# Optimization experiments

Measured on AMD Instinct MI355X. Metric: run time of the kernel, lower is better.

Reference implementation:

```python
import jax, jax.numpy as jnp
import numpy as np

R = 8
EPS = 1e-08
EPSS = 1e-12


def _diff_x(x, r):
    left = x[:, :, r:2 * r + 1]
    middle = x[:, :, 2 * r + 1:] - x[:, :, :-2 * r - 1]
    right = x[:, :, -1:] - x[:, :, -2 * r - 1:-r - 1]
    return jnp.concatenate([left, middle, right], axis=2)


def _diff_y(x, r):
    left = x[:, :, :, r:2 * r + 1]
    middle = x[:, :, :, 2 * r + 1:] - x[:, :, :, :-2 * r - 1]
    right = x[:, :, :, -1:] - x[:, :, :, -2 * r - 1:-r - 1]
    return jnp.concatenate([left, middle, right], axis=3)


def box_filter(x, r):
    # cumsum-based (2r+1)x(2r+1) box sum with clamped borders (matches torch BoxFilter)
    return _diff_y(jnp.cumsum(_diff_x(jnp.cumsum(x, axis=2), r), axis=3), r)


def bilinear_resize(x, H, W):
    # F.interpolate(mode='bilinear', align_corners=True) for NCHW
    n, c, h, w = x.shape
    ys = jnp.linspace(0.0, h - 1.0, H)
    xs = jnp.linspace(0.0, w - 1.0, W)
    y0 = jnp.floor(ys).astype(jnp.int32)
    x0 = jnp.floor(xs).astype(jnp.int32)
    y1 = jnp.minimum(y0 + 1, h - 1)
    x1 = jnp.minimum(x0 + 1, w - 1)
    wy = (ys - y0).astype(x.dtype)[None, None, :, None]
    wx = (xs - x0).astype(x.dtype)[None, None, None, :]
    rows = jnp.take(x, y0, axis=2) * (1.0 - wy) + jnp.take(x, y1, axis=2) * wy
    return jnp.take(rows, x0, axis=3) * (1.0 - wx) + jnp.take(rows, x1, axis=3) * wx


def setup_inputs() -> dict:
    key = jax.random.key(0)
    k1, k2, k3, k4 = jax.random.split(key, 4)
    return {
        "lr_x": jax.random.normal(k1, (4, 3, 256, 256), dtype=jnp.float32),
        "lr_y": jax.random.normal(k2, (4, 3, 256, 256), dtype=jnp.float32),
        "hr_x": jax.random.normal(k3, (4, 3, 1024, 1024), dtype=jnp.float32),
        "l_a": jax.random.uniform(k4, (4, 3, 256, 256), dtype=jnp.float32),
    }


def reference(lr_x, lr_y, hr_x, l_a):
    n, c, h, w = lr_x.shape
    _, _, hh, wh = hr_x.shape
    dt = lr_x.dtype

    N = box_filter(jnp.ones((1, 1, h, w), dtype=dt), R)  # local window counts

    l_a = jnp.abs(l_a) + EPSS
    l_t = l_a / jnp.sum(l_a)

    mean_a = box_filter(l_a) if False else box_filter(l_a, R) / N
    mean_a2xy = box_filter(l_a * l_a * lr_x * lr_y, R) / N
    mean_tax = box_filter(l_t * l_a * lr_x, R) / N
    mean_ay = box_filter(l_a * lr_y, R) / N
    mean_a2x2 = box_filter(l_a * l_a * lr_x * lr_x, R) / N
    mean_ax = box_filter(l_a * lr_x, R) / N

    temp = jnp.abs(mean_a2x2 - N * mean_tax * mean_ax)
    A = (mean_a2xy - N * mean_tax * mean_ay) / (temp + EPS)
    b = (mean_ay - A * mean_ax) / mean_a

    A = box_filter(A, R) / N
    b = box_filter(b, R) / N

    mean_A = bilinear_resize(A, hh, wh)
    mean_b = bilinear_resize(b, hh, wh)
    return (mean_A * hr_x + mean_b).astype(jnp.float32)
```

## Files before the change

kernel.cpp:

```cpp
#include <hip/hip_runtime.h>

#define RAD 8
#define HH 256
#define WW 256
#define NC 12
#define PS (HH*WW)
#define SCALE (255.0f/1023.0f)

#define NREG 68
#define NMID 52
#define NCEN 36
#define INP  69
#define HP   53
#define CP   37
#define HS   (NREG*HP)

__device__ __forceinline__ int swz(int b) { return (b & 7) * 96 + (b >> 3); }

__global__ __launch_bounds__(256) void k_reduce(const float* __restrict__ la,
                                                float* __restrict__ partials) {
    int tid = threadIdx.x;
    __shared__ float ls[4];
    const float4* p4 = (const float4*)la;
    int base = blockIdx.x * 2048 + tid;
    float s = 0.f;
    #pragma unroll
    for (int i = 0; i < 8; i++) {
        float4 v = p4[base + i * 256];
        s += (fabsf(v.x) + 1e-12f) + (fabsf(v.y) + 1e-12f) +
             (fabsf(v.z) + 1e-12f) + (fabsf(v.w) + 1e-12f);
    }
    for (int off = 32; off > 0; off >>= 1) s += __shfl_down(s, off, 64);
    int lane = tid & 63, wid = tid >> 6;
    if (lane == 0) ls[wid] = s;
    __syncthreads();
    if (tid == 0) partials[blockIdx.x] = ls[0] + ls[1] + ls[2] + ls[3];
}

__global__ __launch_bounds__(512, 1) void k_fused(const float* __restrict__ la,
                                                  const float* __restrict__ lx,
                                                  const float* __restrict__ ly,
                                                  const float* __restrict__ hrx,
                                                  const float* __restrict__ partials,
                                                  float* __restrict__ out) {
    __shared__ float sIn[3 * NREG * INP];
    __shared__ float sH[6 * HS];
    __shared__ float sred[8];
    float* inA  = sIn;
    float* inX  = sIn + NREG * INP;
    float* inY  = sIn + 2 * NREG * INP;
    float* Abuf = inA;
    float* Bbuf = inX;
    float* HAb  = inY;
    float* HBb  = inY + NMID * CP;
    float* mAb  = sH;
    float* mBb  = sH + NCEN * CP;

    int tid = threadIdx.x;
    int b  = swz(blockIdx.x);
    int p  = b >> 6;
    int t  = b & 63;
    int ti = t >> 3, tj = t & 7;
    int I0 = ti << 7, J0 = tj << 7;
    int Lr0 = max(0, (I0 * 255) / 1023 - 1);
    int Lc0 = max(0, (J0 * 255) / 1023 - 1);

    {
        float x = (tid < 96) ? partials[tid] : 0.f;
        for (int off = 32; off > 0; off >>= 1) x += __shfl_down(x, off, 64);
        if ((tid & 63) == 0) sred[tid >> 6] = x;
    }

    int r0g = Lr0 - 16, c0g = Lc0 - 16;
    const int plane = p * PS;
    for (unsigned idx = tid; idx < (unsigned)(NREG * NREG); idx += 512u) {
        int r = (int)(idx / 68u), c = (int)(idx % 68u);
        int gr = r0g + r, gc = c0g + c;
        float va = 0.f, vx = 0.f, vy = 0.f;
        if (gr >= 0 && gr < HH && gc >= 0 && gc < WW) {
            int off = plane + gr * WW + gc;
            va = fabsf(la[off]) + 1e-12f;
            vx = lx[off];
            vy = ly[off];
        }
        int w = r * INP + c;
        inA[w] = va; inX[w] = vx; inY[w] = vy;
    }
    __syncthreads();
    float invS = 1.0f / (sred[0] + sred[1] + sred[2] + sred[3] +
                         sred[4] + sred[5] + sred[6] + sred[7]);

    for (unsigned job = tid; job < 272u; job += 512u) {
        int r = (int)(job % 68u), strip = (int)(job / 68u);
        const float* rA = inA + r * INP;
        const float* rX = inX + r * INP;
        const float* rY = inY + r * INP;
        float* w0 = sH + r * HP;
        int c0 = strip * 13;
        float s0 = 0, s1 = 0, s2 = 0, s3 = 0, s4 = 0, s5 = 0;
        #pragma unroll
        for (int c = 0; c < 17; c++) {
            float a = rA[c0 + c], x = rX[c0 + c], y = rY[c0 + c];
            float ax = a * x, ay = a * y;
            s0 += a; s1 += ax; s2 += ay; s3 += a * ax; s4 += ax * ax; s5 += ax * ay;
        }
        w0[c0] = s0; w0[HS + c0] = s1; w0[2 * HS + c0] = s2;
        w0[3 * HS + c0] = s3; w0[4 * HS + c0] = s4; w0[5 * HS + c0] = s5;
        for (int jm = c0 + 1; jm <= c0 + 12; jm++) {
            float a = rA[jm + 16], x = rX[jm + 16], y = rY[jm + 16];
            float ax = a * x, ay = a * y;
            s0 += a; s1 += ax; s2 += ay; s3 += a * ax; s4 += ax * ax; s5 += ax * ay;
            a = rA[jm - 1]; x = rX[jm - 1]; y = rY[jm - 1];
            ax = a * x; ay = a * y;
            s0 -= a; s1 -= ax; s2 -= ay; s3 -= a * ax; s4 -= ax * ax; s5 -= ax * ay;
            w0[jm] = s0; w0[HS + jm] = s1; w0[2 * HS + jm] = s2;
            w0[3 * HS + jm] = s3; w0[4 * HS + jm] = s4; w0[5 * HS + jm] = s5;
        }
    }
    __syncthreads();

    for (unsigned job = tid; job < 208u; job += 512u) {
        int jm = (int)(job % 52u), strip = (int)(job / 52u);
        int gjC = Lc0 - 8 + jm;
        bool cok = (gjC >= 0) && (gjC < WW);
        float cxw = (float)(min(gjC + RAD, WW - 1) - max(gjC - RAD, 0) + 1);
        const float* colp = sH + jm;
        int r0 = strip * 13;
        float s0 = 0, s1 = 0, s2 = 0, s3 = 0, s4 = 0, s5 = 0;
        #pragma unroll
        for (int d = 0; d < 17; d++) {
            int o = (r0 + d) * HP;
            s0 += colp[o];          s1 += colp[HS + o];     s2 += colp[2 * HS + o];
            s3 += colp[3 * HS + o]; s4 += colp[4 * HS + o]; s5 += colp[5 * HS + o];
        }
        for (int im = r0; im < r0 + 13; im++) {
            if (im > r0) {
                int oa = (im + 16) * HP, os = (im - 1) * HP;
                s0 += colp[oa] - colp[os];
                s1 += colp[HS + oa] - colp[HS + os];
                s2 += colp[2 * HS + oa] - colp[2 * HS + os];
                s3 += colp[3 * HS + oa] - colp[3 * HS + os];
                s4 += colp[4 * HS + oa] - colp[4 * HS + os];
                s5 += colp[5 * HS + oa] - colp[5 * HS + os];
            }
            int giR = Lr0 - 8 + im;
            float Av = 0.f, bv = 0.f;
            if (cok && giR >= 0 && giR < HH) {
                float cyw = (float)(min(giR + RAD, HH - 1) - max(giR - RAD, 0) + 1);
                float Nv = cxw * cyw, invN = 1.0f / Nv;
                float m_a = s0 * invN, m_ax = s1 * invN, m_ay = s2 * invN;
                float m_tax = s3 * invN * invS;
                float m_a2x2 = s4 * invN, m_a2xy = s5 * invN;
                float tempv = fabsf(m_a2x2 - Nv * m_tax * m_ax);
                Av = (m_a2xy - Nv * m_tax * m_ay) / (tempv + 1e-8f);
                bv = (m_ay - Av * m_ax) / m_a;
            }
            Abuf[im * HP + jm] = Av;
            Bbuf[im * HP + jm] = bv;
        }
    }
    __syncthreads();

    for (unsigned job = tid; job < 208u; job += 512u) {
        int row   = (int)(job % 52u);
        int which = (int)((job / 52u) & 1u);
        int strip = (int)(job / 104u);
        const float* rp = (which ? Bbuf : Abuf) + row * HP;
        float* dst = (which ? HBb : HAb) + row * CP;
        int c0 = strip * 18;
        float sum = 0.f;
        #pragma unroll
        for (int c = 0; c < 17; c++) sum += rp[c0 + c];
        dst[c0] = sum;
        for (int jc = c0 + 1; jc < c0 + 18; jc++) {
            sum += rp[jc + 16] - rp[jc - 1];
            dst[jc] = sum;
        }
    }
    __syncthreads();

    for (unsigned job = tid; job < 144u; job += 512u) {
        int colc  = (int)(job % 36u);
        int which = (int)((job / 36u) & 1u);
        int strip = (int)(job / 72u);
        const float* src = which ? HBb : HAb;
        float* dst = which ? mBb : mAb;
        int gjC = Lc0 + colc;
        float cxw = (float)(min(gjC + RAD, WW - 1) - max(gjC - RAD, 0) + 1);
        int r0 = strip * 18;
        float sum = 0.f;
        #pragma unroll
        for (int d = 0; d < 17; d++) sum += src[(r0 + d) * CP + colc];
        for (int ic = r0; ic < r0 + 18; ic++) {
            if (ic > r0) sum += src[(ic + 16) * CP + colc] - src[(ic - 1) * CP + colc];
            int giR = Lr0 + ic;
            float cyw = (float)(min(giR + RAD, HH - 1) - max(giR - RAD, 0) + 1);
            dst[ic * CP + colc] = sum / (cxw * cyw);
        }
    }
    __syncthreads();

    {
        int col4 = tid & 31;
        int rb   = tid >> 5;
        int J4 = (J0 >> 2) + col4;
        int Jp = J4 << 2;
        int xb = (int)((float)Jp * SCALE);
        int i1 = min(xb + 1, WW - 1), i2 = min(xb + 2, WW - 1);
        int lxb = xb - Lc0, li1 = i1 - Lc0, li2 = i2 - Lc0;
        float wxv[4]; bool hs[4];
        #pragma unroll
        for (int k = 0; k < 4; k++) {
            float xsk = (float)(Jp + k) * SCALE;
            int x0 = (int)xsk;
            wxv[k] = xsk - (float)x0;
            hs[k] = (x0 > xb);
        }
        const float4* h4 = (const float4*)hrx;
        float4* o4 = (float4*)out;
        int planeHR = p * 262144;
        #pragma unroll
        for (int it = 0; it < 8; it++) {
            int row = (it << 4) + rb;
            int I = I0 + row;
            float ysf = (float)I * SCALE;
            int y0 = (int)ysf;
            float wy = ysf - (float)y0;
            int y1 = min(y0 + 1, HH - 1);
            int ly0 = y0 - Lr0, ly1 = y1 - Lr0;
            const float* a0p = mAb + ly0 * CP;
            const float* a1p = mAb + ly1 * CP;
            const float* b0p = mBb + ly0 * CP;
            const float* b1p = mBb + ly1 * CP;
            float A0a = a0p[lxb], A0b = a0p[li1], A0c = a0p[li2];
            float A1a = a1p[lxb], A1b = a1p[li1], A1c = a1p[li2];
            float B0a = b0p[lxb], B0b = b0p[li1], B0c = b0p[li2];
            float B1a = b1p[lxb], B1b = b1p[li1], B1c = b1p[li2];
            int hidx = planeHR + I * 256 + J4;
            float4 h = h4[hidx];
            float hv[4] = {h.x, h.y, h.z, h.w};
            float ov[4];
            float omwy = 1.0f - wy;
            #pragma unroll
            for (int k = 0; k < 4; k++) {
                bool hb = hs[k];
                float Alo0 = hb ? A0b : A0a, Ahi0 = hb ? A0c : A0b;
                float Alo1 = hb ? A1b : A1a, Ahi1 = hb ? A1c : A1b;
                float Blo0 = hb ? B0b : B0a, Bhi0 = hb ? B0c : B0b;
                float Blo1 = hb ? B1b : B1a, Bhi1 = hb ? B1c : B1b;
                float wx = wxv[k], omwx = 1.0f - wx;
                float Ar0 = Alo0 * omwx + Ahi0 * wx;
                float Ar1 = Alo1 * omwx + Ahi1 * wx;
                float Br0 = Blo0 * omwx + Bhi0 * wx;
                float Br1 = Blo1 * omwx + Bhi1 * wx;
                float Avv = Ar0 * omwy + Ar1 * wy;
                float Bvv = Br0 * omwy + Br1 * wy;
                ov[k] = Avv * hv[k] + Bvv;
            }
            float4 o; o.x = ov[0]; o.y = ov[1]; o.z = ov[2]; o.w = ov[3];
            o4[hidx] = o;
        }
    }
}

extern "C" void kernel_launch(void* const* d_in, const int* in_sizes, int n_in,
                              void* d_out, int out_size, void* d_ws, size_t ws_size,
                              hipStream_t stream) {
    const float* lr_x = (const float*)d_in[0];
    const float* lr_y = (const float*)d_in[1];
    const float* hr_x = (const float*)d_in[2];
    const float* l_a  = (const float*)d_in[3];
    float* partials = (float*)d_ws;

    k_reduce<<<96, 256, 0, stream>>>(l_a, partials);
    k_fused<<<768, 512, 0, stream>>>(l_a, lr_x, lr_y, hr_x, partials, (float*)d_out);
}
```

Before: 155.1 us.

## Split fused kernel into global A/b pass and upsample tile kernel

Computes A and b once per low-res pixel in a separate kernel that writes them to workspace. It uses a wave-shuffle running sum along columns and a sliding vertical window per wavefront. The tile kernel then only loads A/b halos, does the second box filter and the bilinear upsample with 256 threads per block. This removes the redundant halo recomputation of the six first-stage box sums in each tile and the large shared-memory footprint that limited occupancy. The cost is an extra launch and a global round trip for A/b.

```diff
diff --git a/kernel.cpp b/kernel.cpp
--- a/kernel.cpp
+++ b/kernel.cpp
@@ -5,17 +5,23 @@
 #define WW 256
 #define NC 12
 #define PS (HH*WW)
-#define SCALE (255.0f/1023.0f)
-
-#define NREG 68
-#define NMID 52
-#define NCEN 36
-#define INP  69
-#define HP   53
-#define CP   37
-#define HS   (NREG*HP)
-
-__device__ __forceinline__ int swz(int b) { return (b & 7) * 96 + (b >> 3); }
+
+#define NA 52
+#define NM 36
+#define AP 53
+#define CP 37
+
+__device__ __forceinline__ int swz768(int b) { return (b & 7) * 96 + (b >> 3); }
+__device__ __forceinline__ int swz576(int b) { return (b & 7) * 72 + (b >> 3); }
+
+__device__ __forceinline__ float run17(float x) {
+    float s = x + __shfl_up(x, 1, 64);
+    s += __shfl_up(s, 2, 64);
+    s += __shfl_up(s, 4, 64);
+    s += __shfl_up(s, 8, 64);
+    s += __shfl_up(x, 16, 64);
+    return s;
+}
 
 __global__ __launch_bounds__(256) void k_reduce(const float* __restrict__ la,
                                                 float* __restrict__ partials) {
@@ -37,27 +43,90 @@
     if (tid == 0) partials[blockIdx.x] = ls[0] + ls[1] + ls[2] + ls[3];
 }
 
-__global__ __launch_bounds__(512, 1) void k_fused(const float* __restrict__ la,
-                                                  const float* __restrict__ lx,
-                                                  const float* __restrict__ ly,
-                                                  const float* __restrict__ hrx,
-                                                  const float* __restrict__ partials,
-                                                  float* __restrict__ out) {
-    __shared__ float sIn[3 * NREG * INP];
-    __shared__ float sH[6 * HS];
-    __shared__ float sred[8];
-    float* inA  = sIn;
-    float* inX  = sIn + NREG * INP;
-    float* inY  = sIn + 2 * NREG * INP;
-    float* Abuf = inA;
-    float* Bbuf = inX;
-    float* HAb  = inY;
-    float* HBb  = inY + NMID * CP;
-    float* mAb  = sH;
-    float* mBb  = sH + NCEN * CP;
+__global__ __launch_bounds__(256) void k_ab(const float* __restrict__ la,
+                                            const float* __restrict__ lx,
+                                            const float* __restrict__ ly,
+                                            const float* __restrict__ partials,
+                                            float* __restrict__ Ab,
+                                            float* __restrict__ Bb) {
+    int tid = threadIdx.x, lane = tid & 63, wv = tid >> 6;
+    int gw = swz576(blockIdx.x) * 4 + wv;
+    int p  = gw / 192;
+    int r  = gw - p * 192;
+    int s  = r >> 5;
+    int bd = r & 31;
+    int i0 = bd << 3;
+    int C0 = s * 48;
+    int col = C0 - 8 + lane;
+    bool vc = (col >= 0) && (col < WW);
+    int colc = min(max(col, 0), WW - 1);
+    const float* pa = la + p * PS + colc;
+    const float* px = lx + p * PS + colc;
+    const float* py = ly + p * PS + colc;
+
+    float psum = partials[lane] + ((lane < 32) ? partials[lane + 64] : 0.0f);
+    #pragma unroll
+    for (int off = 32; off > 0; off >>= 1) psum += __shfl_xor(psum, off, 64);
+    float invS = 1.0f / psum;
+
+    int  cA  = C0 - 16 + lane;
+    bool vcA = (lane >= 16) && (cA < WW);
+    float cxA = (float)(min(cA + RAD, WW - 1) - max(cA - RAD, 0) + 1);
+
+    float s0 = 0, s1 = 0, s2 = 0, s3 = 0, s4 = 0, s5 = 0;
+    auto accum = [&](int rr, float sg) {
+        float va = 0.f, vx = 0.f, vy = 0.f;
+        if (vc) { int o = rr * WW; va = pa[o]; vx = px[o]; vy = py[o]; }
+        float a  = vc ? (fabsf(va) + 1e-12f) : 0.f;
+        float ax = a * vx, ay = a * vy;
+        s0 = fmaf(sg, a, s0); s1 = fmaf(sg, ax, s1); s2 = fmaf(sg, ay, s2);
+        s3 = fmaf(sg, a * ax, s3); s4 = fmaf(sg, ax * ax, s4); s5 = fmaf(sg, ax * ay, s5);
+    };
+
+    #pragma unroll
+    for (int d = -8; d <= 8; ++d) {
+        int rr = i0 + d;
+        if (rr >= 0 && rr < HH) accum(rr, 1.0f);
+    }
+
+    float* Apl = Ab + p * PS;
+    float* Bpl = Bb + p * PS;
+    #pragma unroll
+    for (int k = 0; k < 8; ++k) {
+        int m = i0 + k;
+        if (k > 0) {
+            int ra = m + 8; if (ra < HH) accum(ra, 1.0f);
+            int rs = m - 9; if (rs >= 0) accum(rs, -1.0f);
+        }
+        float h0 = run17(s0), h1 = run17(s1), h2 = run17(s2),
+              h3 = run17(s3), h4 = run17(s4), h5 = run17(s5);
+        float cy = (float)(min(m + RAD, HH - 1) - max(m - RAD, 0) + 1);
+        float Nv = cxA * cy, invN = 1.0f / Nv;
+        float m_a = h0 * invN, m_ax = h1 * invN, m_ay = h2 * invN;
+        float m_tax = h3 * invN * invS;
+        float m_a2x2 = h4 * invN, m_a2xy = h5 * invN;
+        float tempv = fabsf(m_a2x2 - Nv * m_tax * m_ax);
+        float Av = (m_a2xy - Nv * m_tax * m_ay) / (tempv + 1e-8f);
+        float bv = (m_ay - Av * m_ax) / m_a;
+        if (vcA) {
+            int o = m * WW + cA;
+            Apl[o] = Av;
+            Bpl[o] = bv;
+        }
+    }
+}
+
+__global__ __launch_bounds__(256) void k_tile(const float* __restrict__ Ab,
+                                              const float* __restrict__ Bb,
+                                              const float* __restrict__ hrx,
+                                              float* __restrict__ out) {
+    __shared__ float sA[NA * AP], sB[NA * AP];
+    __shared__ float sHA[NA * CP], sHB[NA * CP];
+    float* mAb = sA;
+    float* mBb = sB;
 
     int tid = threadIdx.x;
-    int b  = swz(blockIdx.x);
+    int b  = swz768(blockIdx.x);
     int p  = b >> 6;
     int t  = b & 63;
     int ti = t >> 3, tj = t & 7;
@@ -65,133 +134,52 @@
     int Lr0 = max(0, (I0 * 255) / 1023 - 1);
     int Lc0 = max(0, (J0 * 255) / 1023 - 1);
 
-    {
-        float x = (tid < 96) ? partials[tid] : 0.f;
-        for (int off = 32; off > 0; off >>= 1) x += __shfl_down(x, off, 64);
-        if ((tid & 63) == 0) sred[tid >> 6] = x;
-    }
-
-    int r0g = Lr0 - 16, c0g = Lc0 - 16;
-    const int plane = p * PS;
-    for (unsigned idx = tid; idx < (unsigned)(NREG * NREG); idx += 512u) {
-        int r = (int)(idx / 68u), c = (int)(idx % 68u);
-        int gr = r0g + r, gc = c0g + c;
-        float va = 0.f, vx = 0.f, vy = 0.f;
+    const float* Apl = Ab + p * PS;
+    const float* Bpl = Bb + p * PS;
+    for (int idx = tid; idx < NA * NA; idx += 256) {
+        int r = idx / NA, c = idx - r * NA;
+        int gr = Lr0 - 8 + r, gc = Lc0 - 8 + c;
+        float av = 0.f, bv = 0.f;
         if (gr >= 0 && gr < HH && gc >= 0 && gc < WW) {
-            int off = plane + gr * WW + gc;
-            va = fabsf(la[off]) + 1e-12f;
-            vx = lx[off];
-            vy = ly[off];
-        }
-        int w = r * INP + c;
-        inA[w] = va; inX[w] = vx; inY[w] = vy;
-    }
-    __syncthreads();
-    float invS = 1.0f / (sred[0] + sred[1] + sred[2] + sred[3] +
-                         sred[4] + sred[5] + sred[6] + sred[7]);
-
-    for (unsigned job = tid; job < 272u; job += 512u) {
-        int r = (int)(job % 68u), strip = (int)(job / 68u);
-        const float* rA = inA + r * INP;
-        const float* rX = inX + r * INP;
-        const float* rY = inY + r * INP;
-        float* w0 = sH + r * HP;
-        int c0 = strip * 13;
-        float s0 = 0, s1 = 0, s2 = 0, s3 = 0, s4 = 0, s5 = 0;
-        #pragma unroll
-        for (int c = 0; c < 17; c++) {
-            float a = rA[c0 + c], x = rX[c0 + c], y = rY[c0 + c];
-            float ax = a * x, ay = a * y;
-            s0 += a; s1 += ax; s2 += ay; s3 += a * ax; s4 += ax * ax; s5 += ax * ay;
-        }
-        w0[c0] = s0; w0[HS + c0] = s1; w0[2 * HS + c0] = s2;
-        w0[3 * HS + c0] = s3; w0[4 * HS + c0] = s4; w0[5 * HS + c0] = s5;
-        for (int jm = c0 + 1; jm <= c0 + 12; jm++) {
-            float a = rA[jm + 16], x = rX[jm + 16], y = rY[jm + 16];
-            float ax = a * x, ay = a * y;
-            s0 += a; s1 += ax; s2 += ay; s3 += a * ax; s4 += ax * ax; s5 += ax * ay;
-            a = rA[jm - 1]; x = rX[jm - 1]; y = rY[jm - 1];
-            ax = a * x; ay = a * y;
-            s0 -= a; s1 -= ax; s2 -= ay; s3 -= a * ax; s4 -= ax * ax; s5 -= ax * ay;
-            w0[jm] = s0; w0[HS + jm] = s1; w0[2 * HS + jm] = s2;
-            w0[3 * HS + jm] = s3; w0[4 * HS + jm] = s4; w0[5 * HS + jm] = s5;
-        }
-    }
-    __syncthreads();
-
-    for (unsigned job = tid; job < 208u; job += 512u) {
-        int jm = (int)(job % 52u), strip = (int)(job / 52u);
-        int gjC = Lc0 - 8 + jm;
-        bool cok = (gjC >= 0) && (gjC < WW);
-        float cxw = (float)(min(gjC + RAD, WW - 1) - max(gjC - RAD, 0) + 1);
-        const float* colp = sH + jm;
-        int r0 = strip * 13;
-        float s0 = 0, s1 = 0, s2 = 0, s3 = 0, s4 = 0, s5 = 0;
-        #pragma unroll
-        for (int d = 0; d < 17; d++) {
-            int o = (r0 + d) * HP;
-            s0 += colp[o];          s1 += colp[HS + o];     s2 += colp[2 * HS + o];
-            s3 += colp[3 * HS + o]; s4 += colp[4 * HS + o]; s5 += colp[5 * HS + o];
-        }
-        for (int im = r0; im < r0 + 13; im++) {
-            if (im > r0) {
-                int oa = (im + 16) * HP, os = (im - 1) * HP;
-                s0 += colp[oa] - colp[os];
-                s1 += colp[HS + oa] - colp[HS + os];
-                s2 += colp[2 * HS + oa] - colp[2 * HS + os];
-                s3 += colp[3 * HS + oa] - colp[3 * HS + os];
-                s4 += colp[4 * HS + oa] - colp[4 * HS + os];
-                s5 += colp[5 * HS + oa] - colp[5 * HS + os];
-            }
-            int giR = Lr0 - 8 + im;
-            float Av = 0.f, bv = 0.f;
-            if (cok && giR >= 0 && giR < HH) {
-                float cyw = (float)(min(giR + RAD, HH - 1) - max(giR - RAD, 0) + 1);
-                float Nv = cxw * cyw, invN = 1.0f / Nv;
-                float m_a = s0 * invN, m_ax = s1 * invN, m_ay = s2 * invN;
-                float m_tax = s3 * invN * invS;
-                float m_a2x2 = s4 * invN, m_a2xy = s5 * invN;
-                float tempv = fabsf(m_a2x2 - Nv * m_tax * m_ax);
-                Av = (m_a2xy - Nv * m_tax * m_ay) / (tempv + 1e-8f);
-                bv = (m_ay - Av * m_ax) / m_a;
-            }
-            Abuf[im * HP + jm] = Av;
-            Bbuf[im * HP + jm] = bv;
-        }
-    }
-    __syncthreads();
-
-    for (unsigned job = tid; job < 208u; job += 512u) {
-        int row   = (int)(job % 52u);
-        int which = (int)((job / 52u) & 1u);
-        int strip = (int)(job / 104u);
-        const float* rp = (which ? Bbuf : Abuf) + row * HP;
-        float* dst = (which ? HBb : HAb) + row * CP;
+            int o = gr * WW + gc;
+            av = Apl[o]; bv = Bpl[o];
+        }
+        sA[r * AP + c] = av;
+        sB[r * AP + c] = bv;
+    }
+    __syncthreads();
+
+    for (int job = tid; job < 208; job += 256) {
+        int row   = job % 52;
+        int which = (job / 52) & 1;
+        int strip = job / 104;
+        const float* rp = (which ? sB : sA) + row * AP;
+        float* dst = (which ? sHB : sHA) + row * CP;
         int c0 = strip * 18;
         float sum = 0.f;
         #pragma unroll
-        for (int c = 0; c < 17; c++) sum += rp[c0 + c];
+        for (int c = 0; c < 17; ++c) sum += rp[c0 + c];
         dst[c0] = sum;
-        for (int jc = c0 + 1; jc < c0 + 18; jc++) {
+        for (int jc = c0 + 1; jc < c0 + 18; ++jc) {
             sum += rp[jc + 16] - rp[jc - 1];
             dst[jc] = sum;
         }
     }
     __syncthreads();
 
-    for (unsigned job = tid; job < 144u; job += 512u) {
-        int colc  = (int)(job % 36u);
-        int which = (int)((job / 36u) & 1u);
-        int strip = (int)(job / 72u);
-        const float* src = which ? HBb : HAb;
+    for (int job = tid; job < 144; job += 256) {
+        int colc  = job % 36;
+        int which = (job / 36) & 1;
+        int strip = job / 72;
+        const float* src = which ? sHB : sHA;
         float* dst = which ? mBb : mAb;
         int gjC = Lc0 + colc;
         float cxw = (float)(min(gjC + RAD, WW - 1) - max(gjC - RAD, 0) + 1);
         int r0 = strip * 18;
         float sum = 0.f;
         #pragma unroll
-        for (int d = 0; d < 17; d++) sum += src[(r0 + d) * CP + colc];
-        for (int ic = r0; ic < r0 + 18; ic++) {
+        for (int d = 0; d < 17; ++d) sum += src[(r0 + d) * CP + colc];
+        for (int ic = r0; ic < r0 + 18; ++ic) {
             if (ic > r0) sum += src[(ic + 16) * CP + colc] - src[(ic - 1) * CP + colc];
             int giR = Lr0 + ic;
             float cyw = (float)(min(giR + RAD, HH - 1) - max(giR - RAD, 0) + 1);
@@ -205,13 +193,14 @@
         int rb   = tid >> 5;
         int J4 = (J0 >> 2) + col4;
         int Jp = J4 << 2;
-        int xb = (int)((float)Jp * SCALE);
+        const float scale = 255.0f / 1023.0f;
+        int xb = (int)((float)Jp * scale);
         int i1 = min(xb + 1, WW - 1), i2 = min(xb + 2, WW - 1);
         int lxb = xb - Lc0, li1 = i1 - Lc0, li2 = i2 - Lc0;
         float wxv[4]; bool hs[4];
         #pragma unroll
         for (int k = 0; k < 4; k++) {
-            float xsk = (float)(Jp + k) * SCALE;
+            float xsk = (float)(Jp + k) * scale;
             int x0 = (int)xsk;
             wxv[k] = xsk - (float)x0;
             hs[k] = (x0 > xb);
@@ -220,10 +209,10 @@
         float4* o4 = (float4*)out;
         int planeHR = p * 262144;
         #pragma unroll
-        for (int it = 0; it < 8; it++) {
-            int row = (it << 4) + rb;
+        for (int it = 0; it < 16; ++it) {
+            int row = (it << 3) + rb;
             int I = I0 + row;
-            float ysf = (float)I * SCALE;
+            float ysf = (float)I * scale;
             int y0 = (int)ysf;
             float wy = ysf - (float)y0;
             int y1 = min(y0 + 1, HH - 1);
@@ -270,8 +259,14 @@
     const float* lr_y = (const float*)d_in[1];
     const float* hr_x = (const float*)d_in[2];
     const float* l_a  = (const float*)d_in[3];
-    float* partials = (float*)d_ws;
+    float* out = (float*)d_out;
+
+    float* ws       = (float*)d_ws;
+    float* partials = ws;
+    float* Ab       = ws + 256;
+    float* Bb       = Ab + NC * PS;
 
     k_reduce<<<96, 256, 0, stream>>>(l_a, partials);
-    k_fused<<<768, 512, 0, stream>>>(l_a, lr_x, lr_y, hr_x, partials, (float*)d_out);
-}
+    k_ab    <<<576, 256, 0, stream>>>(l_a, lr_x, lr_y, partials, Ab, Bb);
+    k_tile  <<<768, 256, 0, stream>>>(Ab, Bb, hr_x, out);
+}
```

Result: faster. 139.4 us (-10.1%).
